# Performance work log

Measured on AMD Instinct MI355X. Metric: run time of the kernel, lower is better.

## Reference

```python
import jax, jax.numpy as jnp
import numpy as np

N_EMBED = 1024
N_HEAD = 16


def setup_inputs() -> dict:
    key = jax.random.key(0)
    k1, k2, k3 = jax.random.split(key, 3)
    B, T, C = 4, 2048, N_EMBED
    x = jax.random.normal(k1, (B, T, C), dtype=jnp.float32)
    # Linear weights stored as [in, out] so forward is x @ W
    scale = 1.0 / np.sqrt(C)
    W_attn = jax.random.normal(k2, (C, 3 * C), dtype=jnp.float32) * scale
    W_proj = jax.random.normal(k3, (C, C), dtype=jnp.float32) * scale
    return {"x": x, "W_attn": W_attn, "W_proj": W_proj}


def reference(x, W_attn, W_proj):
    B, T, C = x.shape
    H = N_HEAD
    D = C // H
    qkv = x @ W_attn  # [B, T, 3C]
    q, k, v = jnp.split(qkv, 3, axis=-1)
    # [B, H, T, D]
    q = q.reshape(B, T, H, D).transpose(0, 2, 1, 3)
    k = k.reshape(B, T, H, D).transpose(0, 2, 1, 3)
    v = v.reshape(B, T, H, D).transpose(0, 2, 1, 3)
    scores = jnp.einsum('bhqd,bhkd->bhqk', q, k) * (1.0 / np.sqrt(D))
    causal = jnp.tril(jnp.ones((T, T), dtype=bool))
    scores = jnp.where(causal, scores, -jnp.inf)
    attn = jax.nn.softmax(scores, axis=-1)
    y = jnp.einsum('bhqk,bhkd->bhqd', attn, v)  # [B, H, T, D]
    y = y.transpose(0, 2, 1, 3).reshape(B, T, C)
    return y @ W_proj
```

## Files before the change

### kernel.cpp

```cpp
#include <hip/hip_runtime.h>

using bf16x8 = __attribute__((ext_vector_type(8))) __bf16;
using f32x4  = __attribute__((ext_vector_type(4))) float;
using f32x16 = __attribute__((ext_vector_type(16))) float;

__device__ __forceinline__ unsigned short f2bf(float f) {
  unsigned u = __builtin_bit_cast(unsigned, f);
  u += 0x7fffu + ((u >> 16) & 1u);
  return (unsigned short)(u >> 16);
}

__device__ __forceinline__ unsigned cvt_pk_bf16(float lo, float hi) {
  unsigned r;
  asm("v_cvt_pk_bf16_f32 %0, %1, %2" : "=v"(r) : "v"(lo), "v"(hi));
  return r;
}

__device__ __forceinline__ void permswap(unsigned &a, unsigned &b) {
  asm("v_permlane32_swap_b32 %0, %1" : "+v"(a), "+v"(b));
}

__device__ __forceinline__ void gload_lds16(const void* g, void* l) {
  __builtin_amdgcn_global_load_lds((const __attribute__((address_space(1))) void*)g,
                                   (__attribute__((address_space(3))) void*)l, 16, 0, 0);
}

__global__ void cvt_bf16_kernel(const float* __restrict__ in,
                                unsigned short* __restrict__ out, int n) {
  int i = (blockIdx.x * blockDim.x + threadIdx.x) * 4;
  if (i < n) {
    float4 f = *(const float4*)(in + i);
    ushort4 o;
    o.x = f2bf(f.x); o.y = f2bf(f.y); o.z = f2bf(f.z); o.w = f2bf(f.w);
    *(ushort4*)(out + i) = o;
  }
}

__global__ void transpose_cvt_kernel(const float* __restrict__ W,
                                     unsigned short* __restrict__ WT, int K, int N) {
  __shared__ float tile[32][33];
  int n0 = blockIdx.x * 32, k0 = blockIdx.y * 32;
  int tx = threadIdx.x, ty = threadIdx.y;
  #pragma unroll
  for (int i = 0; i < 32; i += 8)
    tile[ty + i][tx] = W[(size_t)(k0 + ty + i) * N + (n0 + tx)];
  __syncthreads();
  #pragma unroll
  for (int i = 0; i < 32; i += 8)
    WT[(size_t)(n0 + ty + i) * K + (k0 + tx)] = f2bf(tile[tx][ty + i]);
}

template <int MODE>
__global__ __launch_bounds__(256, 2)
void gemm_bf16(const unsigned short* __restrict__ A,
               const unsigned short* __restrict__ BT,
               float* __restrict__ Cout, int K,
               unsigned short* __restrict__ q_out,
               unsigned short* __restrict__ k_out,
               unsigned short* __restrict__ v_out, int N) {
  __shared__ alignas(16) char smem[32768];
  char* As = smem;
  char* Bs = smem + 16384;
  const int tid = threadIdx.x;
  const int lane = tid & 63, w = tid >> 6;
  const int wm = w >> 1, wn = w & 1;
  const int l15 = lane & 15, l4 = lane >> 4;
  const int bm = blockIdx.y, bn = blockIdx.x;

  f32x4 acc[4][4] = {};

  for (int kt = 0; kt < K; kt += 64) {
    #pragma unroll
    for (int i = 0; i < 4; i++) {
      int row = i * 32 + w * 8 + (lane >> 3);
      int sc = (lane & 7) ^ (row & 7);
      gload_lds16(A + (size_t)(bm * 128 + row) * K + kt + sc * 8, As + i * 4096 + w * 1024);
      gload_lds16(BT + (size_t)(bn * 128 + row) * K + kt + sc * 8, Bs + i * 4096 + w * 1024);
    }
    __syncthreads();
    #pragma unroll
    for (int kk = 0; kk < 2; kk++) {
      bf16x8 af[4], bfr[4];
      #pragma unroll
      for (int mc = 0; mc < 4; mc++) {
        int row = wm * 64 + mc * 16 + l15;
        af[mc] = *(const bf16x8*)(As + row * 128 + (((kk * 4 + l4) ^ (row & 7)) << 4));
      }
      #pragma unroll
      for (int nc = 0; nc < 4; nc++) {
        int row = wn * 64 + nc * 16 + l15;
        bfr[nc] = *(const bf16x8*)(Bs + row * 128 + (((kk * 4 + l4) ^ (row & 7)) << 4));
      }
      #pragma unroll
      for (int mc = 0; mc < 4; mc++)
        #pragma unroll
        for (int nc = 0; nc < 4; nc++)
          acc[mc][nc] = __builtin_amdgcn_mfma_f32_16x16x32_bf16(af[mc], bfr[nc], acc[mc][nc], 0, 0, 0);
    }
    __syncthreads();
  }

  if (MODE == 0 && bn >= 16) {
    unsigned short* tt = (unsigned short*)smem;
    #pragma unroll
    for (int mc = 0; mc < 4; mc++)
      #pragma unroll
      for (int nc = 0; nc < 4; nc++)
        #pragma unroll
        for (int r = 0; r < 4; r++) {
          int ml = wm * 64 + mc * 16 + l4 * 4 + r;
          int nl = wn * 64 + nc * 16 + l15;
          tt[nl * 128 + (ml ^ ((nl & 7) << 3))] = f2bf(acc[mc][nc][r]);
        }
    __syncthreads();
    const int b_ = bm >> 4;
    const int t0 = (bm & 15) * 128;
    const int mm = (tid & 15) * 8;
    #pragma unroll
    for (int it = 0; it < 8; it++) {
      int nl = it * 16 + (tid >> 4);
      int n = bn * 128 + nl;
      int h = (n >> 6) & 15, d = n & 63;
      int4 val = *(const int4*)&tt[nl * 128 + (mm ^ ((nl & 7) << 3))];
      *(int4*)(v_out + ((size_t)(b_ * 16 + h) * 64 + d) * 2048 + t0 + mm) = val;
    }
  } else {
    const float qsc = (MODE == 0 && bn < 8) ? 0.18033688f : 1.0f;
    #pragma unroll
    for (int mc = 0; mc < 4; mc++) {
      #pragma unroll
      for (int nc = 0; nc < 4; nc++) {
        #pragma unroll
        for (int r = 0; r < 4; r++) {
          int m = bm * 128 + wm * 64 + mc * 16 + l4 * 4 + r;
          int n = bn * 128 + wn * 64 + nc * 16 + l15;
          float val = acc[mc][nc][r] * qsc;
          if (MODE == 0) {
            int b = m >> 11, t = m & 2047;
            int which = n >> 10, h = (n >> 6) & 15, d = n & 63;
            unsigned short* dst = (which == 0) ? q_out : k_out;
            dst[(((size_t)(b * 16 + h)) * 2048 + t) * 64 + d] = f2bf(val);
          } else {
            Cout[(size_t)m * N + n] = val;
          }
        }
      }
    }
  }
}

__device__ __forceinline__ void repack_pa(const f32x16 s, bf16x8 &fl, bf16x8 &fh) {
  unsigned p01 = cvt_pk_bf16(s[0], s[1]);
  unsigned p23 = cvt_pk_bf16(s[2], s[3]);
  unsigned p45 = cvt_pk_bf16(s[4], s[5]);
  unsigned p67 = cvt_pk_bf16(s[6], s[7]);
  unsigned p89 = cvt_pk_bf16(s[8], s[9]);
  unsigned pAB = cvt_pk_bf16(s[10], s[11]);
  unsigned pCD = cvt_pk_bf16(s[12], s[13]);
  unsigned pEF = cvt_pk_bf16(s[14], s[15]);
  permswap(p01, p45);
  permswap(p23, p67);
  permswap(p89, pCD);
  permswap(pAB, pEF);
  uint4 f0, f1;
  f0.x = p01; f0.y = p23; f0.z = p45; f0.w = p67;
  f1.x = p89; f1.y = pAB; f1.z = pCD; f1.w = pEF;
  fl = __builtin_bit_cast(bf16x8, f0);
  fh = __builtin_bit_cast(bf16x8, f1);
}

__global__ __launch_bounds__(256, 4)
void attn_kernel(const unsigned short* __restrict__ q,
                 const unsigned short* __restrict__ k,
                 const unsigned short* __restrict__ vT,
                 unsigned short* __restrict__ att) {
  __shared__ alignas(16) char smem[32768];

  const int bid = blockIdx.x;
  const int qt = 15 - (bid >> 6);
  const int bh = bid & 63;
  const int tid = threadIdx.x;
  const int lane = tid & 63, w = tid >> 6;
  const int l31 = lane & 31, hi = lane >> 5;
  const size_t base = (size_t)bh * 2048 * 64;

  bf16x8 qf[4];
  const int qwb = qt * 128 + w * 32;
  const int qrow = qwb + l31;
  #pragma unroll
  for (int ks = 0; ks < 4; ks++)
    qf[ks] = *(const bf16x8*)(q + base + (size_t)qrow * 64 + ks * 16 + hi * 8);
  asm volatile("" :: "v"(qf[0]), "v"(qf[1]), "v"(qf[2]), "v"(qf[3]));

  const char* kb4[4];
  #pragma unroll
  for (int ks = 0; ks < 4; ks++)
    kb4[ks] = smem + l31 * 128 + (((2 * ks + hi) ^ (l31 & 7)) << 4);

  const int srow = w * 8 + (lane >> 3);
  const int sc8 = ((lane & 7) ^ (srow & 7)) * 8;

  f32x16 o0 = {}, o1 = {}, lacc = {};
  const int qmax = qwb + 31;
  const int ntiles = 2 * qt + 2;

  uint4 onesw;
  onesw.x = 0x3F803F80u; onesw.y = 0x3F803F80u; onesw.z = 0x3F803F80u; onesw.w = 0x3F803F80u;
  const bf16x8 onesv = __builtin_bit_cast(bf16x8, onesw);

  {
    const unsigned short* kp = k + base + srow * 64 + sc8;
    gload_lds16(kp,         smem + w * 1024);
    gload_lds16(kp + 2048,  smem + 4096 + w * 1024);
    const unsigned short* vp = vT + base + (size_t)srow * 2048 + sc8;
    gload_lds16(vp,          smem + 16384 + w * 1024);
    gload_lds16(vp + 65536,  smem + 16384 + 4096 + w * 1024);
  }
  const unsigned short* kq1 = k + base + srow * 64 + sc8 + 4096;
  const unsigned short* kq2 = kq1 + 4096;
  const unsigned short* vq1 = vT + base + (size_t)srow * 2048 + sc8 + 64;
  const unsigned short* vq2 = vq1 + 64;

#define COMPUTE_TILE(BUF, KBASE)                                               \
  do {                                                                         \
    const int kbase_ = (KBASE);                                                \
    if (kbase_ <= qmax) {                                                      \
      f32x16 s0 = {}, s1 = {};                                                 \
      __builtin_amdgcn_s_setprio(1);                                           \
      _Pragma("unroll")                                                        \
      for (int ks = 0; ks < 4; ks++) {                                         \
        bf16x8 k0 = *(const bf16x8*)(kb4[ks] + (BUF));                         \
        bf16x8 k1 = *(const bf16x8*)(kb4[ks] + (BUF) + 4096);                  \
        s0 = __builtin_amdgcn_mfma_f32_32x32x16_bf16(k0, qf[ks], s0, 0, 0, 0); \
        s1 = __builtin_amdgcn_mfma_f32_32x32x16_bf16(k1, qf[ks], s1, 0, 0, 0); \
      }                                                                        \
      __builtin_amdgcn_s_setprio(0);                                           \
      if (kbase_ + 63 > qwb) {                                                 \
        _Pragma("unroll")                                                      \
        for (int r = 0; r < 16; r++) {                                         \
          int crow = (r & 3) + 8 * (r >> 2) + 4 * hi;                          \
          if (kbase_ + crow > qrow) s0[r] = -1e30f;                            \
          if (kbase_ + 32 + crow > qrow) s1[r] = -1e30f;                       \
        }                                                                      \
      }                                                                        \
      _Pragma("unroll")                                                        \
      for (int r = 0; r < 16; r++) {                                           \
        float t0_ = s0[r], t1_ = s1[r];                                        \
        asm("v_exp_f32 %0, %0" : "+v"(t0_));                                   \
        asm("v_exp_f32 %0, %0" : "+v"(t1_));                                   \
        s0[r] = t0_; s1[r] = t1_;                                              \
      }                                                                        \
      bf16x8 pa[4];                                                            \
      repack_pa(s0, pa[0], pa[1]);                                             \
      repack_pa(s1, pa[2], pa[3]);                                             \
      __builtin_amdgcn_s_setprio(1);                                           \
      _Pragma("unroll")                                                        \
      for (int ks = 0; ks < 4; ks++) {                                         \
        bf16x8 vf0 = *(const bf16x8*)(kb4[ks] + 16384 + (BUF));                \
        bf16x8 vf1 = *(const bf16x8*)(kb4[ks] + 16384 + (BUF) + 4096);         \
        o0 = __builtin_amdgcn_mfma_f32_32x32x16_bf16(pa[ks], vf0, o0, 0, 0, 0);\
        o1 = __builtin_amdgcn_mfma_f32_32x32x16_bf16(pa[ks], vf1, o1, 0, 0, 0);\
        lacc = __builtin_amdgcn_mfma_f32_32x32x16_bf16(pa[ks], onesv, lacc, 0, 0, 0);\
      }                                                                        \
      __builtin_amdgcn_s_setprio(0);                                           \
    }                                                                          \
  } while (0)

  for (int t = 0; t < ntiles; t += 2) {
    gload_lds16(kq1,         smem + 8192 + w * 1024);
    gload_lds16(kq1 + 2048,  smem + 8192 + 4096 + w * 1024);
    gload_lds16(vq1,         smem + 16384 + 8192 + w * 1024);
    gload_lds16(vq1 + 65536, smem + 16384 + 8192 + 4096 + w * 1024);
    kq1 += 8192; vq1 += 128;
    asm volatile("s_waitcnt vmcnt(4)" ::: "memory");
    __builtin_amdgcn_s_barrier();
    __builtin_amdgcn_sched_barrier(0);
    COMPUTE_TILE(0, t * 64);
    __builtin_amdgcn_s_barrier();
    __builtin_amdgcn_sched_barrier(0);

    if (t + 2 < ntiles) {
      gload_lds16(kq2,         smem + w * 1024);
      gload_lds16(kq2 + 2048,  smem + 4096 + w * 1024);
      gload_lds16(vq2,         smem + 16384 + w * 1024);
      gload_lds16(vq2 + 65536, smem + 16384 + 4096 + w * 1024);
      kq2 += 8192; vq2 += 128;
      asm volatile("s_waitcnt vmcnt(4)" ::: "memory");
    } else {
      asm volatile("s_waitcnt vmcnt(0)" ::: "memory");
    }
    __builtin_amdgcn_s_barrier();
    __builtin_amdgcn_sched_barrier(0);
    COMPUTE_TILE(8192, t * 64 + 64);
    __builtin_amdgcn_s_barrier();
    __builtin_amdgcn_sched_barrier(0);
  }
#undef COMPUTE_TILE

  const int b_ = bh >> 4, h = bh & 15;
  #pragma unroll
  for (int r = 0; r < 16; r++) {
    int crow = (r & 3) + 8 * (r >> 2) + 4 * hi;
    float li = 1.0f / lacc[r];
    int t = qt * 128 + w * 32 + crow;
    size_t rb = ((size_t)(b_ * 2048 + t)) * 1024 + h * 64;
    att[rb + l31] = f2bf(o0[r] * li);
    att[rb + 32 + l31] = f2bf(o1[r] * li);
  }
}

extern "C" void kernel_launch(void* const* d_in, const int* in_sizes, int n_in,
                              void* d_out, int out_size, void* d_ws, size_t ws_size,
                              hipStream_t stream) {
  const float* x  = (const float*)d_in[0];
  const float* Wa = (const float*)d_in[1];
  const float* Wp = (const float*)d_in[2];
  float* out = (float*)d_out;
  char* ws = (char*)d_ws;

  unsigned short* xb  = (unsigned short*)(ws);
  unsigned short* WaT = (unsigned short*)(ws + 16777216);
  unsigned short* WpT = (unsigned short*)(ws + 23068672);
  unsigned short* qb  = (unsigned short*)(ws + 25165824);
  unsigned short* kb  = (unsigned short*)(ws + 41943040);
  unsigned short* vtb = (unsigned short*)(ws + 58720256);
  unsigned short* att = xb;

  cvt_bf16_kernel<<<8192, 256, 0, stream>>>(x, xb, 8388608);
  dim3 tb(32, 8);
  transpose_cvt_kernel<<<dim3(96, 32), tb, 0, stream>>>(Wa, WaT, 1024, 3072);
  transpose_cvt_kernel<<<dim3(32, 32), tb, 0, stream>>>(Wp, WpT, 1024, 1024);

  gemm_bf16<0><<<dim3(24, 64), 256, 0, stream>>>(xb, WaT, nullptr, 1024, qb, kb, vtb, 3072);

  attn_kernel<<<1024, 256, 0, stream>>>(qb, kb, vtb, att);

  gemm_bf16<1><<<dim3(8, 64), 256, 0, stream>>>(att, WpT, out, 1024, nullptr, nullptr, nullptr, 1024);
}
```

Before: 152.2 us.

## Use 256x256 double-buffered pipelined GEMM for QKV projection

Replaces the 128x128 QKV GEMM with a dedicated 256x256-tile kernel that uses 512 threads and 128KB of LDS double buffering. Global-to-LDS loads for the next k-tile are interleaved between MFMA groups, with setprio and explicit waitcnt. The larger tile raises arithmetic intensity and overlaps loads with compute. The cost is one block per CU and a grid of only 384 blocks, which may underfill the 256 CUs in the last wave. The output projection GEMM is split into its own simplified kernel.

```diff
diff --git a/kernel.cpp b/kernel.cpp
--- a/kernel.cpp
+++ b/kernel.cpp
@@ -50,14 +50,161 @@
     WT[(size_t)(n0 + ty + i) * K + (k0 + tx)] = f2bf(tile[tx][ty + i]);
 }
 
-template <int MODE>
+__global__ __launch_bounds__(512, 1)
+void gemm256_qkv(const unsigned short* __restrict__ A,
+                 const unsigned short* __restrict__ BT,
+                 unsigned short* __restrict__ q_out,
+                 unsigned short* __restrict__ k_out,
+                 unsigned short* __restrict__ v_out) {
+  constexpr int K = 1024;
+  __shared__ alignas(16) char smem[131072];
+
+  const int tid = threadIdx.x;
+  const int lane = tid & 63, w = tid >> 6;
+  const int wm = w >> 2, wn = w & 3;
+  const int l15 = lane & 15, l4 = lane >> 4;
+  const int bm = blockIdx.y, bn = blockIdx.x;
+
+  const int srow = w * 8 + (lane >> 3);
+  const int schunk = ((lane & 7) ^ (srow & 7)) * 8;
+  const unsigned short* pa = A + (size_t)(bm * 256 + srow) * K + schunk;
+  const unsigned short* pb = BT + (size_t)(bn * 256 + srow) * K + schunk;
+  const int sdst = w * 1024;
+
+  f32x4 acc[8][4] = {};
+
+#define GLA(j2, nxt, tcol) gload_lds16(pa + (size_t)(j2) * 64 * K + (tcol), \
+                                       smem + (nxt) * 32768 + (j2) * 8192 + sdst)
+#define GLB(j2, nxt, tcol) gload_lds16(pb + (size_t)(j2) * 64 * K + (tcol), \
+                                       smem + 65536 + (nxt) * 32768 + (j2) * 8192 + sdst)
+
+  GLA(0, 0, 0); GLA(1, 0, 0); GLA(2, 0, 0); GLA(3, 0, 0);
+  GLB(0, 0, 0); GLB(1, 0, 0); GLB(2, 0, 0); GLB(3, 0, 0);
+
+  for (int t = 0; t < 16; t++) {
+    const int cur = t & 1, nxt = cur ^ 1;
+    const int tcol = (t + 1) * 64;
+    const bool more = (t < 15);
+
+    __builtin_amdgcn_s_barrier();
+    if (more) { GLA(0, nxt, tcol); GLA(1, nxt, tcol); }
+    if (more) asm volatile("s_waitcnt vmcnt(2)" ::: "memory");
+    else      asm volatile("s_waitcnt vmcnt(0)" ::: "memory");
+    __builtin_amdgcn_s_barrier();
+    __builtin_amdgcn_sched_barrier(0);
+
+    const char* Ab = smem + cur * 32768;
+    const char* Bb = smem + 65536 + cur * 32768;
+
+    bf16x8 bf[4][2];
+    #pragma unroll
+    for (int nf = 0; nf < 4; nf++) {
+      int rowb = wn * 64 + nf * 16 + l15;
+      #pragma unroll
+      for (int kc = 0; kc < 2; kc++)
+        bf[nf][kc] = *(const bf16x8*)(Bb + rowb * 128 + (((kc * 4 + l4) ^ (rowb & 7)) << 4));
+    }
+    bf16x8 a0[2][2], a1[2][2];
+    #pragma unroll
+    for (int i = 0; i < 2; i++) {
+      int rowa = wm * 128 + i * 16 + l15;
+      #pragma unroll
+      for (int kc = 0; kc < 2; kc++)
+        a0[i][kc] = *(const bf16x8*)(Ab + rowa * 128 + (((kc * 4 + l4) ^ (rowa & 7)) << 4));
+    }
+
+#define LDA(dst, mfb)                                                            \
+    _Pragma("unroll")                                                            \
+    for (int i = 0; i < 2; i++) {                                                \
+      int rowa = wm * 128 + ((mfb) + i) * 16 + l15;                              \
+      _Pragma("unroll")                                                          \
+      for (int kc = 0; kc < 2; kc++)                                             \
+        dst[i][kc] = *(const bf16x8*)(Ab + rowa * 128 + (((kc * 4 + l4) ^ (rowa & 7)) << 4)); \
+    }
+#define MFMA16(mb, af)                                                           \
+    __builtin_amdgcn_s_setprio(1);                                               \
+    _Pragma("unroll")                                                            \
+    for (int m = 0; m < 2; m++)                                                  \
+      _Pragma("unroll")                                                          \
+      for (int nf = 0; nf < 4; nf++) {                                           \
+        acc[(mb) + m][nf] = __builtin_amdgcn_mfma_f32_16x16x32_bf16(af[m][0], bf[nf][0], acc[(mb) + m][nf], 0, 0, 0); \
+        acc[(mb) + m][nf] = __builtin_amdgcn_mfma_f32_16x16x32_bf16(af[m][1], bf[nf][1], acc[(mb) + m][nf], 0, 0, 0); \
+      }                                                                          \
+    __builtin_amdgcn_s_setprio(0);                                               \
+    __builtin_amdgcn_sched_barrier(0);
+
+    LDA(a1, 2);
+    if (more) { GLA(2, nxt, tcol); GLA(3, nxt, tcol); }
+    MFMA16(0, a0);
+    LDA(a0, 4);
+    if (more) { GLB(0, nxt, tcol); GLB(1, nxt, tcol); }
+    MFMA16(2, a1);
+    LDA(a1, 6);
+    if (more) { GLB(2, nxt, tcol); GLB(3, nxt, tcol); }
+    MFMA16(4, a0);
+    MFMA16(6, a1);
+#undef LDA
+#undef MFMA16
+  }
+#undef GLA
+#undef GLB
+
+  if (bn < 8) {
+    const float qsc = (bn < 4) ? 0.18033688f : 1.0f;
+    unsigned short* dst = (bn < 4) ? q_out : k_out;
+    #pragma unroll
+    for (int mf = 0; mf < 8; mf++) {
+      #pragma unroll
+      for (int nf = 0; nf < 4; nf++) {
+        #pragma unroll
+        for (int r = 0; r < 4; r++) {
+          int m = bm * 256 + wm * 128 + mf * 16 + l4 * 4 + r;
+          int n = bn * 256 + wn * 64 + nf * 16 + l15;
+          int h = (n >> 6) & 15, d = n & 63;
+          dst[((size_t)((m >> 11) * 16 + h) * 2048 + (m & 2047)) * 64 + d] =
+              f2bf(acc[mf][nf][r] * qsc);
+        }
+      }
+    }
+  } else {
+    unsigned short* tt = (unsigned short*)smem;
+    const int b_ = bm >> 3;
+    #pragma unroll
+    for (int ch = 0; ch < 2; ch++) {
+      __syncthreads();
+      if ((wn >> 1) == ch) {
+        #pragma unroll
+        for (int mf = 0; mf < 8; mf++)
+          #pragma unroll
+          for (int nf = 0; nf < 4; nf++)
+            #pragma unroll
+            for (int r = 0; r < 4; r++) {
+              int row_l = wm * 128 + mf * 16 + l4 * 4 + r;
+              int cl = (wn & 1) * 64 + nf * 16 + l15;
+              tt[cl * 256 + (row_l ^ ((cl & 7) << 3))] = f2bf(acc[mf][nf][r]);
+            }
+      }
+      __syncthreads();
+      #pragma unroll
+      for (int p = 0; p < 8; p++) {
+        int idx = p * 512 + tid;
+        int cl = idx >> 5;
+        int row0 = (idx & 31) * 8;
+        int4 val = *(const int4*)&tt[cl * 256 + (row0 ^ ((cl & 7) << 3))];
+        int n = bn * 256 + ch * 128 + cl;
+        int vh = n - 2048;
+        int h = vh >> 6, d = vh & 63;
+        int t0 = (bm & 7) * 256 + row0;
+        *(int4*)(v_out + ((size_t)(b_ * 16 + h) * 64 + d) * 2048 + t0) = val;
+      }
+    }
+  }
+}
+
 __global__ __launch_bounds__(256, 2)
-void gemm_bf16(const unsigned short* __restrict__ A,
-               const unsigned short* __restrict__ BT,
-               float* __restrict__ Cout, int K,
-               unsigned short* __restrict__ q_out,
-               unsigned short* __restrict__ k_out,
-               unsigned short* __restrict__ v_out, int N) {
+void gemm128_out(const unsigned short* __restrict__ A,
+                 const unsigned short* __restrict__ BT,
+                 float* __restrict__ Cout, int K, int N) {
   __shared__ alignas(16) char smem[32768];
   char* As = smem;
   char* Bs = smem + 16384;
@@ -100,53 +247,16 @@
     __syncthreads();
   }
 
-  if (MODE == 0 && bn >= 16) {
-    unsigned short* tt = (unsigned short*)smem;
-    #pragma unroll
-    for (int mc = 0; mc < 4; mc++)
-      #pragma unroll
-      for (int nc = 0; nc < 4; nc++)
-        #pragma unroll
-        for (int r = 0; r < 4; r++) {
-          int ml = wm * 64 + mc * 16 + l4 * 4 + r;
-          int nl = wn * 64 + nc * 16 + l15;
-          tt[nl * 128 + (ml ^ ((nl & 7) << 3))] = f2bf(acc[mc][nc][r]);
-        }
-    __syncthreads();
-    const int b_ = bm >> 4;
-    const int t0 = (bm & 15) * 128;
-    const int mm = (tid & 15) * 8;
-    #pragma unroll
-    for (int it = 0; it < 8; it++) {
-      int nl = it * 16 + (tid >> 4);
-      int n = bn * 128 + nl;
-      int h = (n >> 6) & 15, d = n & 63;
-      int4 val = *(const int4*)&tt[nl * 128 + (mm ^ ((nl & 7) << 3))];
-      *(int4*)(v_out + ((size_t)(b_ * 16 + h) * 64 + d) * 2048 + t0 + mm) = val;
-    }
-  } else {
-    const float qsc = (MODE == 0 && bn < 8) ? 0.18033688f : 1.0f;
-    #pragma unroll
-    for (int mc = 0; mc < 4; mc++) {
-      #pragma unroll
-      for (int nc = 0; nc < 4; nc++) {
-        #pragma unroll
-        for (int r = 0; r < 4; r++) {
-          int m = bm * 128 + wm * 64 + mc * 16 + l4 * 4 + r;
-          int n = bn * 128 + wn * 64 + nc * 16 + l15;
-          float val = acc[mc][nc][r] * qsc;
-          if (MODE == 0) {
-            int b = m >> 11, t = m & 2047;
-            int which = n >> 10, h = (n >> 6) & 15, d = n & 63;
-            unsigned short* dst = (which == 0) ? q_out : k_out;
-            dst[(((size_t)(b * 16 + h)) * 2048 + t) * 64 + d] = f2bf(val);
-          } else {
-            Cout[(size_t)m * N + n] = val;
-          }
-        }
-      }
-    }
-  }
+  #pragma unroll
+  for (int mc = 0; mc < 4; mc++)
+    #pragma unroll
+    for (int nc = 0; nc < 4; nc++)
+      #pragma unroll
+      for (int r = 0; r < 4; r++) {
+        int m = bm * 128 + wm * 64 + mc * 16 + l4 * 4 + r;
+        int n = bn * 128 + wn * 64 + nc * 16 + l15;
+        Cout[(size_t)m * N + n] = acc[mc][nc][r];
+      }
 }
 
 __device__ __forceinline__ void repack_pa(const f32x16 s, bf16x8 &fl, bf16x8 &fh) {
@@ -331,9 +441,9 @@
   transpose_cvt_kernel<<<dim3(96, 32), tb, 0, stream>>>(Wa, WaT, 1024, 3072);
   transpose_cvt_kernel<<<dim3(32, 32), tb, 0, stream>>>(Wp, WpT, 1024, 1024);
 
-  gemm_bf16<0><<<dim3(24, 64), 256, 0, stream>>>(xb, WaT, nullptr, 1024, qb, kb, vtb, 3072);
+  gemm256_qkv<<<dim3(12, 32), 512, 0, stream>>>(xb, WaT, qb, kb, vtb);
 
   attn_kernel<<<1024, 256, 0, stream>>>(qb, kb, vtb, att);
 
-  gemm_bf16<1><<<dim3(8, 64), 256, 0, stream>>>(att, WpT, out, 1024, nullptr, nullptr, nullptr, 1024);
-}
+  gemm128_out<<<dim3(8, 64), 256, 0, stream>>>(att, WpT, out, 1024, 1024);
+}
```

Result: no change. 154.5 us (+1.5%).
